# Performance work log

Measured on AMD Instinct MI355X. Metric: run time of the kernel, lower is better.

The kernel has to match this reference:

```python
import jax, jax.numpy as jnp
import numpy as np
from jax import lax

T, B, I, H, O = 512, 64, 512, 1024, 512

def setup_inputs() -> dict:
    key = jax.random.key(0)
    ks = jax.random.split(key, 7)
    s_ih = 1.0 / np.sqrt(H)
    return {
        "X": jax.random.normal(ks[0], (T, B, I), dtype=jnp.float32),
        "W_ih": jax.random.uniform(ks[1], (4 * H, I), minval=-s_ih, maxval=s_ih, dtype=jnp.float32),
        "W_hh": jax.random.uniform(ks[2], (4 * H, H), minval=-s_ih, maxval=s_ih, dtype=jnp.float32),
        "b_ih": jax.random.uniform(ks[3], (4 * H,), minval=-s_ih, maxval=s_ih, dtype=jnp.float32),
        "b_hh": jax.random.uniform(ks[4], (4 * H,), minval=-s_ih, maxval=s_ih, dtype=jnp.float32),
        "W_ho": jax.random.uniform(ks[5], (O, H), minval=-s_ih, maxval=s_ih, dtype=jnp.float32),
        "b_ho": jax.random.uniform(ks[6], (O,), minval=-s_ih, maxval=s_ih, dtype=jnp.float32),
    }

def reference(X, W_ih, W_hh, b_ih, b_hh, W_ho, b_ho):
    # X: [T, B, I]; PyTorch LSTMCell gate order: i, f, g, o
    Bsz = X.shape[1]
    Hd = W_hh.shape[1]
    h0 = jnp.zeros((Bsz, Hd), dtype=X.dtype)
    c0 = jnp.zeros((Bsz, Hd), dtype=X.dtype)
    # Precompute input projections for all timesteps in one big GEMM: [T,B,4H]
    Xp = jnp.einsum('tbi,gi->tbg', X, W_ih) + b_ih + b_hh

    def step(carry, xp):
        h, c = carry
        gates = xp + h @ W_hh.T  # [B, 4H]
        i, f, g, o = jnp.split(gates, 4, axis=-1)
        c = jax.nn.sigmoid(f) * c + jax.nn.sigmoid(i) * jnp.tanh(g)
        h = jax.nn.sigmoid(o) * jnp.tanh(c)
        return (h, c), None

    (h, c), _ = lax.scan(step, (h0, c0), Xp)
    return h @ W_ho.T + b_ho
```

## Files before the change

### kernel.cpp

```cpp
#include <hip/hip_runtime.h>
#include <hip/hip_bf16.h>

#define T_STEPS 512
#define BATCH   64
#define IDIM    512
#define HDIM    1024
#define ODIM    512
#define NWG     256
#define TPB     512
#define TPB2    256
#define JS      16
#define BGRP    16

typedef __bf16 bf16_t;
typedef bf16_t bf16x8 __attribute__((ext_vector_type(8)));
typedef float  f32x4  __attribute__((ext_vector_type(4)));
typedef unsigned short u16;
typedef unsigned int   u32;
typedef u16 u16x8 __attribute__((ext_vector_type(8)));

#define HBUF_U32 65536
#define FLG_U32  8192
#define XB_U16_OFF (2 * (HBUF_U32 + FLG_U32))

__device__ __forceinline__ float sigmoidf_fast(float x) {
  return 1.0f / (1.0f + __expf(-x));
}
__device__ __forceinline__ float tanhf_fast(float x) {
  float ax = fabsf(x);
  float e  = __expf(-2.0f * ax);
  return copysignf((1.0f - e) / (1.0f + e), x);
}

__global__ void k_init(u32* w) {
  int i = blockIdx.x * blockDim.x + threadIdx.x;
  for (int idx = i; idx < HBUF_U32 + FLG_U32; idx += gridDim.x * blockDim.x) w[idx] = 0u;
}

__global__ __launch_bounds__(TPB2) void k_xcvt(const float* __restrict__ X,
                                               u16* __restrict__ Xb) {
  size_t i = ((size_t)blockIdx.x * TPB2 + threadIdx.x) * 8;
  f32x4 a = *(const f32x4*)(X + i);
  f32x4 b = *(const f32x4*)(X + i + 4);
  u16x8 o;
  o[0] = __builtin_bit_cast(u16, (bf16_t)a[0]);
  o[1] = __builtin_bit_cast(u16, (bf16_t)a[1]);
  o[2] = __builtin_bit_cast(u16, (bf16_t)a[2]);
  o[3] = __builtin_bit_cast(u16, (bf16_t)a[3]);
  o[4] = __builtin_bit_cast(u16, (bf16_t)b[0]);
  o[5] = __builtin_bit_cast(u16, (bf16_t)b[1]);
  o[6] = __builtin_bit_cast(u16, (bf16_t)b[2]);
  o[7] = __builtin_bit_cast(u16, (bf16_t)b[3]);
  *(u16x8*)(Xb + i) = o;
}

__device__ __forceinline__ bf16x8 cvt8(const float* src) {
  f32x4 u = *(const f32x4*)src;
  f32x4 v = *(const f32x4*)(src + 4);
  bf16x8 t;
  t[0] = (bf16_t)u[0]; t[1] = (bf16_t)u[1]; t[2] = (bf16_t)u[2]; t[3] = (bf16_t)u[3];
  t[4] = (bf16_t)v[0]; t[5] = (bf16_t)v[1]; t[6] = (bf16_t)v[2]; t[7] = (bf16_t)v[3];
  return t;
}

#define MFA(CT, AF, WI) \
  acc[CT] = __builtin_amdgcn_mfma_f32_16x16x32_bf16((AF), wf[(WI)*4+(CT)], acc[CT], 0, 0, 0)

#define GLDH(DST, PTR, OFFB) \
  asm volatile("global_load_dwordx4 %0, %1, off offset:" OFFB " sc0 sc1" : "=v"(DST) : "v"(PTR))

#define GWS 20

__global__ __launch_bounds__(TPB, 2) void k_lstm(
    const u16* __restrict__ Xb, const float* __restrict__ Wih,
    const float* __restrict__ Whh, const float* __restrict__ bih,
    const float* __restrict__ bhh, u16* __restrict__ hbuf,
    u32* __restrict__ flg) {
  __shared__ float gw[8][64][GWS];

  const int wg   = blockIdx.x;
  const int grp  = wg >> 6;
  const int widx = wg & 63;
  const int tid  = threadIdx.x;
  const int w    = tid >> 6;
  const int lane = tid & 63;
  const int am   = lane & 15;
  const int kg   = lane >> 4;

  bf16x8 wf[24];
  #pragma unroll
  for (int ct = 0; ct < 4; ++ct) {
    int gr = ct * HDIM + widx * JS + am;
    #pragma unroll
    for (int i = 0; i < 2; ++i)
      wf[i * 4 + ct] = cvt8(Wih + (size_t)gr * IDIM + (w + 8 * i) * 32 + kg * 8);
    #pragma unroll
    for (int i = 2; i < 6; ++i)
      wf[i * 4 + ct] = cvt8(Whh + (size_t)gr * HDIM + (w + 8 * i) * 32 + kg * 8 - IDIM);
  }

  u32* myflag = (lane < 8)
    ? flg + ((size_t)(grp * 64 + 2 * w + (lane & 1) + 16 * (lane >> 1)) * 32)
    : flg;

  const int ebl = tid >> 4;
  const int ej  = tid & 15;
  float bias[4];
  #pragma unroll
  for (int g = 0; g < 4; ++g) {
    int r = g * HDIM + widx * JS + ej;
    bias[g] = bih[r] + bhh[r];
  }
  float c = 0.f;

  f32x4 acc[4];

  auto xphase = [&](int tt) {
    const u16* xb = Xb + ((size_t)tt * BATCH + grp * BGRP + am) * IDIM + w * 32 + kg * 8;
    #pragma unroll
    for (int i = 0; i < 2; ++i) {
      bf16x8 xa = *(const bf16x8*)(xb + i * 256);
      MFA(0, xa, i); MFA(1, xa, i); MFA(2, xa, i); MFA(3, xa, i);
    }
  };

  #pragma unroll
  for (int ct = 0; ct < 4; ++ct) acc[ct] = (f32x4){0.f, 0.f, 0.f, 0.f};
  xphase(0);

  int cur = 0;
  for (int t = 0; t < T_STEPS; ++t) {
    bf16x8 h0, h1, h2, h3;
    const u16* hb0 = hbuf + (size_t)cur * BATCH * HDIM
                   + (size_t)(grp * BGRP + am) * HDIM + w * 32 + kg * 8;
    GLDH(h0, hb0, "0");
    GLDH(h1, hb0, "512");
    GLDH(h2, hb0, "1024");
    GLDH(h3, hb0, "1536");
    __builtin_amdgcn_sched_barrier(0);

    asm volatile("s_waitcnt vmcnt(2)" ::: "memory");
    __builtin_amdgcn_sched_barrier(0);
    MFA(0, h0, 2); MFA(1, h0, 2); MFA(2, h0, 2); MFA(3, h0, 2);
    MFA(0, h1, 3); MFA(1, h1, 3); MFA(2, h1, 3); MFA(3, h1, 3);

    asm volatile("s_waitcnt vmcnt(0)" ::: "memory");
    __builtin_amdgcn_sched_barrier(0);
    MFA(0, h2, 4); MFA(1, h2, 4); MFA(2, h2, 4); MFA(3, h2, 4);
    MFA(0, h3, 5); MFA(1, h3, 5); MFA(2, h3, 5); MFA(3, h3, 5);

    #pragma unroll
    for (int ct = 0; ct < 4; ++ct)
      *(f32x4*)&gw[w][ct * 16 + am][kg * 4] = acc[ct];
    __syncthreads();

    if (tid < 256) {
      float s0 = 0.f, s1 = 0.f, s2 = 0.f, s3 = 0.f;
      #pragma unroll
      for (int ww = 0; ww < 8; ++ww) {
        s0 += gw[ww][ej][ebl];
        s1 += gw[ww][16 + ej][ebl];
        s2 += gw[ww][32 + ej][ebl];
        s3 += gw[ww][48 + ej][ebl];
      }
      float pi = s0 + bias[0], pf = s1 + bias[1];
      float pg = s2 + bias[2], po = s3 + bias[3];
      c = sigmoidf_fast(pf) * c + sigmoidf_fast(pi) * tanhf_fast(pg);
      float h = sigmoidf_fast(po) * tanhf_fast(c);
      u16 hu = __builtin_bit_cast(u16, (bf16_t)h);
      u16* hp = hbuf + (size_t)(cur ^ 1) * BATCH * HDIM
              + (size_t)(grp * BGRP + ebl) * HDIM + widx * JS + ej;
      asm volatile("global_store_short %0, %1, off sc0 sc1"
                   :: "v"(hp), "v"((u32)hu) : "memory");
    }
    __syncthreads();

    if (t != T_STEPS - 1) {
      if (tid == 0) {
        u32 fv = (u32)(t + 1);
        u32* fp = flg + (size_t)(grp * 64 + widx) * 32;
        asm volatile("global_store_dword %0, %1, off sc0 sc1"
                     :: "v"(fp), "v"(fv) : "memory");
      }

      #pragma unroll
      for (int ct = 0; ct < 4; ++ct) acc[ct] = (f32x4){0.f, 0.f, 0.f, 0.f};
      xphase(t + 1);

      {
        const u32 tgt = (u32)(t + 1);
        while (true) {
          u32 v = (lane < 8)
            ? __hip_atomic_load(myflag, __ATOMIC_RELAXED, __HIP_MEMORY_SCOPE_AGENT)
            : tgt;
          if (__all((int)(v >= tgt))) break;
          __builtin_amdgcn_s_sleep(1);
        }
      }
      __builtin_amdgcn_sched_barrier(0);
    }
    cur ^= 1;
  }
}

__global__ __launch_bounds__(TPB2) void k_out(
    const u16* __restrict__ hfin, const float* __restrict__ Who,
    const float* __restrict__ bho, float* __restrict__ out) {
  int gid = blockIdx.x * TPB2 + threadIdx.x;
  int b   = gid & 63;
  int oc  = gid >> 6;
  const u16* hrow = hfin + b * HDIM;
  const float* wrow = Who + oc * HDIM;
  float s = bho[oc];
  for (int k = 0; k < HDIM; k += 8) {
    bf16x8 hv = *(const bf16x8*)(hrow + k);
    f32x4 w0 = *(const f32x4*)(wrow + k);
    f32x4 w1 = *(const f32x4*)(wrow + k + 4);
    s += (float)hv[0] * w0[0] + (float)hv[1] * w0[1] + (float)hv[2] * w0[2] + (float)hv[3] * w0[3]
       + (float)hv[4] * w1[0] + (float)hv[5] * w1[1] + (float)hv[6] * w1[2] + (float)hv[7] * w1[3];
  }
  out[b * ODIM + oc] = s;
}

extern "C" void kernel_launch(void* const* d_in, const int* in_sizes, int n_in,
                              void* d_out, int out_size, void* d_ws, size_t ws_size,
                              hipStream_t stream) {
  const float* X   = (const float*)d_in[0];
  const float* Wih = (const float*)d_in[1];
  const float* Whh = (const float*)d_in[2];
  const float* bih = (const float*)d_in[3];
  const float* bhh = (const float*)d_in[4];
  const float* Who = (const float*)d_in[5];
  const float* bho = (const float*)d_in[6];

  u32* ws32 = (u32*)d_ws;
  u16* hbuf = (u16*)d_ws;
  u32* flg  = ws32 + HBUF_U32;
  u16* Xb   = (u16*)d_ws + XB_U16_OFF;

  k_init<<<64, TPB2, 0, stream>>>(ws32);
  k_xcvt<<<(T_STEPS * BATCH * IDIM) / (TPB2 * 8), TPB2, 0, stream>>>(X, Xb);
  k_lstm<<<NWG, TPB, 0, stream>>>(Xb, Wih, Whh, bih, bhh, hbuf, flg);
  k_out<<<(BATCH * ODIM) / TPB2, TPB2, 0, stream>>>(hbuf, Who, bho, (float*)d_out);
}
```

Before: 1.452 ms.

## Replace per-step block barrier with per-wave flags and double-buffered LDS

Drops the second __syncthreads per timestep. Each of the four epilogue waves now publishes its own readiness flag once its h stores have drained, and consumers poll all four flags per producer workgroup (32 lanes). Double-buffering the LDS gate-reduction array lets the next step's partial sums be written without waiting for the previous reduction to finish. The x-projection MFMAs of the next step run before the flag poll. The cost is four times as many flag loads per poll, one extra LDS buffer, and a flag store per wave instead of per block.

```diff
diff --git a/kernel.cpp b/kernel.cpp
--- a/kernel.cpp
+++ b/kernel.cpp
@@ -20,7 +20,7 @@
 typedef u16 u16x8 __attribute__((ext_vector_type(8)));
 
 #define HBUF_U32 65536
-#define FLG_U32  8192
+#define FLG_U32  32768
 #define XB_U16_OFF (2 * (HBUF_U32 + FLG_U32))
 
 __device__ __forceinline__ float sigmoidf_fast(float x) {
@@ -76,7 +76,7 @@
     const float* __restrict__ Whh, const float* __restrict__ bih,
     const float* __restrict__ bhh, u16* __restrict__ hbuf,
     u32* __restrict__ flg) {
-  __shared__ float gw[8][64][GWS];
+  __shared__ float gw[2][8][64][GWS];
 
   const int wg   = blockIdx.x;
   const int grp  = wg >> 6;
@@ -99,9 +99,13 @@
       wf[i * 4 + ct] = cvt8(Whh + (size_t)gr * HDIM + (w + 8 * i) * 32 + kg * 8 - IDIM);
   }
 
-  u32* myflag = (lane < 8)
-    ? flg + ((size_t)(grp * 64 + 2 * w + (lane & 1) + 16 * (lane >> 1)) * 32)
-    : flg;
+  u32* myflag;
+  {
+    int j = lane >> 2, v = lane & 3;
+    int wp = 2 * w + (j & 1) + 16 * (j >> 1);
+    myflag = flg + ((size_t)((grp * 64 + wp) * 4 + v) * 32);
+  }
+  u32* ownflag = flg + ((size_t)((grp * 64 + widx) * 4 + w) * 32);
 
   const int ebl = tid >> 4;
   const int ej  = tid & 15;
@@ -128,8 +132,20 @@
   for (int ct = 0; ct < 4; ++ct) acc[ct] = (f32x4){0.f, 0.f, 0.f, 0.f};
   xphase(0);
 
-  int cur = 0;
+  int cur = 0, buf = 0;
   for (int t = 0; t < T_STEPS; ++t) {
+    if (t > 0) {
+      const u32 tgt = (u32)t;
+      while (true) {
+        u32 v = (lane < 32)
+          ? __hip_atomic_load(myflag, __ATOMIC_RELAXED, __HIP_MEMORY_SCOPE_AGENT)
+          : tgt;
+        if (__all((int)(v >= tgt))) break;
+        __builtin_amdgcn_s_sleep(1);
+      }
+      __builtin_amdgcn_sched_barrier(0);
+    }
+
     bf16x8 h0, h1, h2, h3;
     const u16* hb0 = hbuf + (size_t)cur * BATCH * HDIM
                    + (size_t)(grp * BGRP + am) * HDIM + w * 32 + kg * 8;
@@ -151,17 +167,17 @@
 
     #pragma unroll
     for (int ct = 0; ct < 4; ++ct)
-      *(f32x4*)&gw[w][ct * 16 + am][kg * 4] = acc[ct];
+      *(f32x4*)&gw[buf][w][ct * 16 + am][kg * 4] = acc[ct];
     __syncthreads();
 
     if (tid < 256) {
       float s0 = 0.f, s1 = 0.f, s2 = 0.f, s3 = 0.f;
       #pragma unroll
       for (int ww = 0; ww < 8; ++ww) {
-        s0 += gw[ww][ej][ebl];
-        s1 += gw[ww][16 + ej][ebl];
-        s2 += gw[ww][32 + ej][ebl];
-        s3 += gw[ww][48 + ej][ebl];
+        s0 += gw[buf][ww][ej][ebl];
+        s1 += gw[buf][ww][16 + ej][ebl];
+        s2 += gw[buf][ww][32 + ej][ebl];
+        s3 += gw[buf][ww][48 + ej][ebl];
       }
       float pi = s0 + bias[0], pf = s1 + bias[1];
       float pg = s2 + bias[2], po = s3 + bias[3];
@@ -172,34 +188,22 @@
               + (size_t)(grp * BGRP + ebl) * HDIM + widx * JS + ej;
       asm volatile("global_store_short %0, %1, off sc0 sc1"
                    :: "v"(hp), "v"((u32)hu) : "memory");
-    }
-    __syncthreads();
+      if (t != T_STEPS - 1) {
+        asm volatile("s_waitcnt vmcnt(0)" ::: "memory");
+        if (lane == 0) {
+          u32 fv = (u32)(t + 1);
+          asm volatile("global_store_dword %0, %1, off sc0 sc1"
+                       :: "v"(ownflag), "v"(fv) : "memory");
+        }
+      }
+    }
 
     if (t != T_STEPS - 1) {
-      if (tid == 0) {
-        u32 fv = (u32)(t + 1);
-        u32* fp = flg + (size_t)(grp * 64 + widx) * 32;
-        asm volatile("global_store_dword %0, %1, off sc0 sc1"
-                     :: "v"(fp), "v"(fv) : "memory");
-      }
-
       #pragma unroll
       for (int ct = 0; ct < 4; ++ct) acc[ct] = (f32x4){0.f, 0.f, 0.f, 0.f};
       xphase(t + 1);
-
-      {
-        const u32 tgt = (u32)(t + 1);
-        while (true) {
-          u32 v = (lane < 8)
-            ? __hip_atomic_load(myflag, __ATOMIC_RELAXED, __HIP_MEMORY_SCOPE_AGENT)
-            : tgt;
-          if (__all((int)(v >= tgt))) break;
-          __builtin_amdgcn_s_sleep(1);
-        }
-      }
-      __builtin_amdgcn_sched_barrier(0);
-    }
-    cur ^= 1;
+    }
+    cur ^= 1; buf ^= 1;
   }
 }
 
```

After: 2.051 ms. +41.2%, slower.

## Replace flag-based step barrier with step-tagged hidden-state words polled directly

Applied to the files above, without the earlier changes.

Each hidden value is now stored as a 32-bit word carrying the bf16 value in the low half and the timestep tag in the high half. Consumers poll the hidden-state loads themselves until every tag matches, so the separate flag store and flag spin loop go away. This is meant to cut the per-step synchronization latency (flag write, flag poll, then data load) down to a single load-and-check. In exchange the hidden buffer doubles in size, each step reads twice as many bytes, and the tag check and repacking add ALU work.

```diff
diff --git a/kernel.cpp b/kernel.cpp
--- a/kernel.cpp
+++ b/kernel.cpp
@@ -18,10 +18,10 @@
 typedef unsigned short u16;
 typedef unsigned int   u32;
 typedef u16 u16x8 __attribute__((ext_vector_type(8)));
-
-#define HBUF_U32 65536
-#define FLG_U32  8192
-#define XB_U16_OFF (2 * (HBUF_U32 + FLG_U32))
+typedef u32 u32x4 __attribute__((ext_vector_type(4)));
+
+#define HBUF2_U32 (2 * BATCH * HDIM)
+#define XB_U16_OFF (2 * HBUF2_U32)
 
 __device__ __forceinline__ float sigmoidf_fast(float x) {
   return 1.0f / (1.0f + __expf(-x));
@@ -34,7 +34,7 @@
 
 __global__ void k_init(u32* w) {
   int i = blockIdx.x * blockDim.x + threadIdx.x;
-  for (int idx = i; idx < HBUF_U32 + FLG_U32; idx += gridDim.x * blockDim.x) w[idx] = 0u;
+  for (int idx = i; idx < HBUF2_U32; idx += gridDim.x * blockDim.x) w[idx] = 0u;
 }
 
 __global__ __launch_bounds__(TPB2) void k_xcvt(const float* __restrict__ X,
@@ -55,7 +55,7 @@
 }
 
 __device__ __forceinline__ bf16x8 cvt8(const float* src) {
-  f32x4 u = *(const f32x4*)src;
+  f32x4 u = *(const f32x4*)(src);
   f32x4 v = *(const f32x4*)(src + 4);
   bf16x8 t;
   t[0] = (bf16_t)u[0]; t[1] = (bf16_t)u[1]; t[2] = (bf16_t)u[2]; t[3] = (bf16_t)u[3];
@@ -66,16 +66,30 @@
 #define MFA(CT, AF, WI) \
   acc[CT] = __builtin_amdgcn_mfma_f32_16x16x32_bf16((AF), wf[(WI)*4+(CT)], acc[CT], 0, 0, 0)
 
-#define GLDH(DST, PTR, OFFB) \
+#define PLD(DST, PTR, OFFB) \
   asm volatile("global_load_dwordx4 %0, %1, off offset:" OFFB " sc0 sc1" : "=v"(DST) : "v"(PTR))
 
 #define GWS 20
+
+__device__ __forceinline__ bf16x8 pack8(u32x4 a, u32x4 b) {
+  u32x4 r;
+  r[0] = (a[0] & 0xFFFFu) | (a[1] << 16);
+  r[1] = (a[2] & 0xFFFFu) | (a[3] << 16);
+  r[2] = (b[0] & 0xFFFFu) | (b[1] << 16);
+  r[3] = (b[2] & 0xFFFFu) | (b[3] << 16);
+  return __builtin_bit_cast(bf16x8, r);
+}
+__device__ __forceinline__ int tags_ok(u32x4 a, u32x4 b, u32 tag) {
+  return (a[0] >> 16) == tag && (a[1] >> 16) == tag &&
+         (a[2] >> 16) == tag && (a[3] >> 16) == tag &&
+         (b[0] >> 16) == tag && (b[1] >> 16) == tag &&
+         (b[2] >> 16) == tag && (b[3] >> 16) == tag;
+}
 
 __global__ __launch_bounds__(TPB, 2) void k_lstm(
     const u16* __restrict__ Xb, const float* __restrict__ Wih,
     const float* __restrict__ Whh, const float* __restrict__ bih,
-    const float* __restrict__ bhh, u16* __restrict__ hbuf,
-    u32* __restrict__ flg) {
+    const float* __restrict__ bhh, u32* __restrict__ hbuf) {
   __shared__ float gw[8][64][GWS];
 
   const int wg   = blockIdx.x;
@@ -99,10 +113,6 @@
       wf[i * 4 + ct] = cvt8(Whh + (size_t)gr * HDIM + (w + 8 * i) * 32 + kg * 8 - IDIM);
   }
 
-  u32* myflag = (lane < 8)
-    ? flg + ((size_t)(grp * 64 + 2 * w + (lane & 1) + 16 * (lane >> 1)) * 32)
-    : flg;
-
   const int ebl = tid >> 4;
   const int ej  = tid & 15;
   float bias[4];
@@ -130,24 +140,38 @@
 
   int cur = 0;
   for (int t = 0; t < T_STEPS; ++t) {
-    bf16x8 h0, h1, h2, h3;
-    const u16* hb0 = hbuf + (size_t)cur * BATCH * HDIM
-                   + (size_t)(grp * BGRP + am) * HDIM + w * 32 + kg * 8;
-    GLDH(h0, hb0, "0");
-    GLDH(h1, hb0, "512");
-    GLDH(h2, hb0, "1024");
-    GLDH(h3, hb0, "1536");
+    const u32* hb = hbuf + (size_t)cur * BATCH * HDIM
+                  + (size_t)(grp * BGRP + am) * HDIM + w * 32 + kg * 8;
+    u32x4 d0a, d0b, d1a, d1b, d2a, d2b, d3a, d3b;
+    {
+      const u32 tag = (u32)t;
+      int ok0 = 0, ok1 = 0, ok2 = 0, ok3 = 0;
+      while (true) {
+        if (!ok0) { PLD(d0a, hb, "0");    PLD(d0b, hb, "16");   }
+        if (!ok1) { PLD(d1a, hb, "1024"); PLD(d1b, hb, "1040"); }
+        if (!ok2) { PLD(d2a, hb, "2048"); PLD(d2b, hb, "2064"); }
+        if (!ok3) { PLD(d3a, hb, "3072"); PLD(d3b, hb, "3088"); }
+        asm volatile("s_waitcnt vmcnt(0)" ::: "memory");
+        if (!ok0) ok0 = __all(tags_ok(d0a, d0b, tag));
+        if (!ok1) ok1 = __all(tags_ok(d1a, d1b, tag));
+        if (!ok2) ok2 = __all(tags_ok(d2a, d2b, tag));
+        if (!ok3) ok3 = __all(tags_ok(d3a, d3b, tag));
+        if (ok0 & ok1 & ok2 & ok3) break;
+        __builtin_amdgcn_s_sleep(1);
+      }
+    }
     __builtin_amdgcn_sched_barrier(0);
 
-    asm volatile("s_waitcnt vmcnt(2)" ::: "memory");
-    __builtin_amdgcn_sched_barrier(0);
-    MFA(0, h0, 2); MFA(1, h0, 2); MFA(2, h0, 2); MFA(3, h0, 2);
-    MFA(0, h1, 3); MFA(1, h1, 3); MFA(2, h1, 3); MFA(3, h1, 3);
-
-    asm volatile("s_waitcnt vmcnt(0)" ::: "memory");
-    __builtin_amdgcn_sched_barrier(0);
-    MFA(0, h2, 4); MFA(1, h2, 4); MFA(2, h2, 4); MFA(3, h2, 4);
-    MFA(0, h3, 5); MFA(1, h3, 5); MFA(2, h3, 5); MFA(3, h3, 5);
+    {
+      bf16x8 h0 = pack8(d0a, d0b);
+      bf16x8 h1 = pack8(d1a, d1b);
+      MFA(0, h0, 2); MFA(1, h0, 2); MFA(2, h0, 2); MFA(3, h0, 2);
+      MFA(0, h1, 3); MFA(1, h1, 3); MFA(2, h1, 3); MFA(3, h1, 3);
+      bf16x8 h2 = pack8(d2a, d2b);
+      bf16x8 h3 = pack8(d3a, d3b);
+      MFA(0, h2, 4); MFA(1, h2, 4); MFA(2, h2, 4); MFA(3, h2, 4);
+      MFA(0, h3, 5); MFA(1, h3, 5); MFA(2, h3, 5); MFA(3, h3, 5);
+    }
 
     #pragma unroll
     for (int ct = 0; ct < 4; ++ct)
@@ -168,56 +192,40 @@
       c = sigmoidf_fast(pf) * c + sigmoidf_fast(pi) * tanhf_fast(pg);
       float h = sigmoidf_fast(po) * tanhf_fast(c);
       u16 hu = __builtin_bit_cast(u16, (bf16_t)h);
-      u16* hp = hbuf + (size_t)(cur ^ 1) * BATCH * HDIM
+      u32 word = ((u32)(t + 1) << 16) | (u32)hu;
+      u32* hp = hbuf + (size_t)(cur ^ 1) * BATCH * HDIM
               + (size_t)(grp * BGRP + ebl) * HDIM + widx * JS + ej;
-      asm volatile("global_store_short %0, %1, off sc0 sc1"
-                   :: "v"(hp), "v"((u32)hu) : "memory");
+      asm volatile("global_store_dword %0, %1, off sc0 sc1"
+                   :: "v"(hp), "v"(word) : "memory");
     }
     __syncthreads();
 
     if (t != T_STEPS - 1) {
-      if (tid == 0) {
-        u32 fv = (u32)(t + 1);
-        u32* fp = flg + (size_t)(grp * 64 + widx) * 32;
-        asm volatile("global_store_dword %0, %1, off sc0 sc1"
-                     :: "v"(fp), "v"(fv) : "memory");
-      }
-
       #pragma unroll
       for (int ct = 0; ct < 4; ++ct) acc[ct] = (f32x4){0.f, 0.f, 0.f, 0.f};
       xphase(t + 1);
-
-      {
-        const u32 tgt = (u32)(t + 1);
-        while (true) {
-          u32 v = (lane < 8)
-            ? __hip_atomic_load(myflag, __ATOMIC_RELAXED, __HIP_MEMORY_SCOPE_AGENT)
-            : tgt;
-          if (__all((int)(v >= tgt))) break;
-          __builtin_amdgcn_s_sleep(1);
-        }
-      }
-      __builtin_amdgcn_sched_barrier(0);
     }
     cur ^= 1;
   }
 }
 
 __global__ __launch_bounds__(TPB2) void k_out(
-    const u16* __restrict__ hfin, const float* __restrict__ Who,
+    const u32* __restrict__ hfin, const float* __restrict__ Who,
     const float* __restrict__ bho, float* __restrict__ out) {
   int gid = blockIdx.x * TPB2 + threadIdx.x;
   int b   = gid & 63;
   int oc  = gid >> 6;
-  const u16* hrow = hfin + b * HDIM;
+  const u32* hrow = hfin + b * HDIM;
   const float* wrow = Who + oc * HDIM;
   float s = bho[oc];
-  for (int k = 0; k < HDIM; k += 8) {
-    bf16x8 hv = *(const bf16x8*)(hrow + k);
-    f32x4 w0 = *(const f32x4*)(wrow + k);
-    f32x4 w1 = *(const f32x4*)(wrow + k + 4);
-    s += (float)hv[0] * w0[0] + (float)hv[1] * w0[1] + (float)hv[2] * w0[2] + (float)hv[3] * w0[3]
-       + (float)hv[4] * w1[0] + (float)hv[5] * w1[1] + (float)hv[6] * w1[2] + (float)hv[7] * w1[3];
+  for (int k = 0; k < HDIM; k += 4) {
+    u32x4 hv = *(const u32x4*)(hrow + k);
+    f32x4 wv = *(const f32x4*)(wrow + k);
+    #pragma unroll
+    for (int q = 0; q < 4; ++q) {
+      float hf = (float)__builtin_bit_cast(bf16_t, (u16)(hv[q] & 0xFFFFu));
+      s += hf * wv[q];
+    }
   }
   out[b * ODIM + oc] = s;
 }
@@ -233,13 +241,11 @@
   const float* Who = (const float*)d_in[5];
   const float* bho = (const float*)d_in[6];
 
-  u32* ws32 = (u32*)d_ws;
-  u16* hbuf = (u16*)d_ws;
-  u32* flg  = ws32 + HBUF_U32;
+  u32* hbuf = (u32*)d_ws;
   u16* Xb   = (u16*)d_ws + XB_U16_OFF;
 
-  k_init<<<64, TPB2, 0, stream>>>(ws32);
+  k_init<<<64, TPB2, 0, stream>>>(hbuf);
   k_xcvt<<<(T_STEPS * BATCH * IDIM) / (TPB2 * 8), TPB2, 0, stream>>>(X, Xb);
-  k_lstm<<<NWG, TPB, 0, stream>>>(Xb, Wih, Whh, bih, bhh, hbuf, flg);
+  k_lstm<<<NWG, TPB, 0, stream>>>(Xb, Wih, Whh, bih, bhh, hbuf);
   k_out<<<(BATCH * ODIM) / TPB2, TPB2, 0, stream>>>(hbuf, Who, bho, (float*)d_out);
 }
```

Measured after the change: 2.055 ms. 1.41x slower.
